# Kernel optimization log

Hardware: AMD Instinct MI355X
Metric: run time of the kernel (lower is better)

Reference implementation:

```python
import jax, jax.numpy as jnp
import numpy as np

B, C, H, W = 4, 256, 64, 64
C8 = C // 8  # q/k projection dim = 32

def setup_inputs() -> dict:
    key = jax.random.key(0)
    ks = jax.random.split(key, 6)
    s = 0.02
    return {
        "x": jax.random.normal(ks[0], (B, C, H, W), dtype=jnp.float32),
        "wq": jax.random.normal(ks[1], (C8, C), dtype=jnp.float32) * s,
        "bq": jnp.zeros((C8,), dtype=jnp.float32),
        "wk": jax.random.normal(ks[2], (C8, C), dtype=jnp.float32) * s,
        "bk": jnp.zeros((C8,), dtype=jnp.float32),
        "wv": jax.random.normal(ks[3], (C, C), dtype=jnp.float32) * s,
        "bv": jnp.zeros((C,), dtype=jnp.float32),
        "wo": jax.random.normal(ks[4], (C, C), dtype=jnp.float32) * s,
        "bo": jnp.zeros((C,), dtype=jnp.float32),
        "scale": jnp.zeros((1,), dtype=jnp.float32),
    }

def reference(x, wq, bq, wk, bk, wv, bv, wo, bo, scale):
    b, c, h, w = x.shape
    n = h * w
    xf = x.reshape(b, c, n)  # (B, C, N)
    # 1x1 convs are channel-mixing GEMMs
    q = jnp.einsum('oc,bcn->bon', wq, xf) + bq[None, :, None]  # (B, C8, N)
    k = jnp.einsum('oc,bcn->bon', wk, xf) + bk[None, :, None]  # (B, C8, N)
    v = jnp.einsum('oc,bcn->bon', wv, xf) + bv[None, :, None]  # (B, C,  N)
    inv_sqrt = 1.0 / jnp.sqrt(jnp.asarray(c // 8, dtype=x.dtype))
    scores = jnp.einsum('bon,bom->bnm', q, k) * inv_sqrt  # (B, N, N): query n, key m
    attn = jax.nn.softmax(scores, axis=-1)
    # torch: bmm(value, attn^T) -> attended[:, :, n] = sum_m v[:, :, m] * attn[n, m]
    attended = jnp.einsum('bcm,bnm->bcn', v, attn)  # (B, C, N)
    out = jnp.einsum('oc,bcn->bon', wo, attended) + bo[None, :, None]
    out = out.reshape(b, c, h, w)
    return x + scale[0] * out
```

## Files before the change

### kernel.cpp

```cpp
#include <hip/hip_runtime.h>
#include <stdint.h>

#define B_ 4
#define C_ 256
#define C8_ 32
#define N_ 4096
#define LOG2E 1.4426950408889634f
#define INV_SQRT32 0.17677669529663689f
#define QSCALE (INV_SQRT32 * LOG2E)

typedef __bf16 bf16x8 __attribute__((ext_vector_type(8)));
typedef float f32x16 __attribute__((ext_vector_type(16)));
typedef unsigned int uint4v __attribute__((ext_vector_type(4)));

__device__ __forceinline__ uint16_t f2bf(float f) {
  uint32_t u = __builtin_bit_cast(uint32_t, f);
  return (uint16_t)((u + 0x7FFFu + ((u >> 16) & 1u)) >> 16);
}
__device__ __forceinline__ uint32_t pack2bf(float a, float b) {
  uint32_t ua = __builtin_bit_cast(uint32_t, a);
  uint32_t ub = __builtin_bit_cast(uint32_t, b);
  ua = (ua + 0x7FFFu + ((ua >> 16) & 1u)) >> 16;
  ub = (ub + 0x7FFFu + ((ub >> 16) & 1u)) & 0xFFFF0000u;
  return ua | ub;
}
__device__ __forceinline__ bf16x8 load_bf8(const uint16_t* p) {
  uint4v u = *(const uint4v*)p;
  return __builtin_bit_cast(bf16x8, u);
}
__device__ __forceinline__ f32x16 mfma32(bf16x8 a, bf16x8 b, f32x16 c) {
  return __builtin_amdgcn_mfma_f32_32x32x16_bf16(a, b, c, 0, 0, 0);
}
__device__ __forceinline__ f32x16 mfma32_f8(long a, long b, f32x16 c) {
  return __builtin_amdgcn_mfma_f32_32x32x16_fp8_fp8(a, b, c, 0, 0, 0);
}

__device__ __forceinline__ void pack_p_fp8(const float* P, int h, long& pa, long& pb) {
  uint32_t w0 = __builtin_amdgcn_cvt_pk_fp8_f32(P[0], P[1], 0, false);
  w0 = __builtin_amdgcn_cvt_pk_fp8_f32(P[2], P[3], w0, true);
  uint32_t w1 = __builtin_amdgcn_cvt_pk_fp8_f32(P[4], P[5], 0, false);
  w1 = __builtin_amdgcn_cvt_pk_fp8_f32(P[6], P[7], w1, true);
  uint32_t w2 = __builtin_amdgcn_cvt_pk_fp8_f32(P[8], P[9], 0, false);
  w2 = __builtin_amdgcn_cvt_pk_fp8_f32(P[10], P[11], w2, true);
  uint32_t w3 = __builtin_amdgcn_cvt_pk_fp8_f32(P[12], P[13], 0, false);
  w3 = __builtin_amdgcn_cvt_pk_fp8_f32(P[14], P[15], w3, true);
  uint32_t s0 = h ? w0 : w1;
  uint32_t s1 = h ? w2 : w3;
  uint32_t r0 = (uint32_t)__shfl_xor((int)s0, 32, 64);
  uint32_t r1 = (uint32_t)__shfl_xor((int)s1, 32, 64);
  uint32_t a0lo = h ? r0 : w0, a0hi = h ? w1 : r0;
  uint32_t a1lo = h ? r1 : w2, a1hi = h ? w3 : r1;
  pa = (long)(((uint64_t)a0hi << 32) | a0lo);
  pb = (long)(((uint64_t)a1hi << 32) | a1lo);
}

__global__ void k_wcast(const float* __restrict__ wq, const float* __restrict__ wk,
                        const float* __restrict__ wv, const float* __restrict__ wo,
                        uint16_t* __restrict__ wqb, uint16_t* __restrict__ wkb,
                        uint16_t* __restrict__ wvb, uint16_t* __restrict__ wob) {
  int i = blockIdx.x * 256 + threadIdx.x;
  if (i < 8192) {
    int o = i >> 8, c = i & 255;
    wqb[((size_t)(c >> 3) * 32 + o) * 8 + (c & 7)] = f2bf(wq[i]);
  } else if (i < 16384) {
    int j = i - 8192; int o = j >> 8, c = j & 255;
    wkb[((size_t)(c >> 3) * 32 + o) * 8 + (c & 7)] = f2bf(wk[j]);
  } else if (i < 81920) {
    int j = i - 16384; int o = j >> 8, c = j & 255;
    wvb[((size_t)(c >> 3) * 256 + o) * 8 + (c & 7)] = f2bf(wv[j]);
  } else {
    int j = i - 81920; int o = j >> 8, c = j & 255;
    wob[((size_t)(c >> 3) * 256 + o) * 8 + (c & 7)] = f2bf(wo[j]);
  }
}

__global__ __launch_bounds__(320) void k_proj_qkv(
    const float* __restrict__ x,
    const uint16_t* __restrict__ wqb, const float* __restrict__ bq,
    const uint16_t* __restrict__ wkb, const float* __restrict__ bk,
    const uint16_t* __restrict__ wvb, const float* __restrict__ bv,
    uint16_t* __restrict__ Qb, uint16_t* __restrict__ Kt, uint8_t* __restrict__ V8) {
  __shared__ uint4v xTv[32 * 32];
  int b = blockIdx.y;
  int n0 = blockIdx.x * 32;
  int tid = threadIdx.x;
  uint16_t* xT = (uint16_t*)xTv;

  if (tid < 256) {
    int r = tid >> 3;
    int l4 = (tid & 7) * 4;
#pragma unroll
    for (int p = 0; p < 8; p++) {
      int c = p * 32 + r;
      float4 v = *(const float4*)(x + ((size_t)b * C_ + c) * N_ + n0 + l4);
      int cg = c >> 3, cj = c & 7;
      xT[(cg * 32 + l4 + 0) * 8 + cj] = f2bf(v.x);
      xT[(cg * 32 + l4 + 1) * 8 + cj] = f2bf(v.y);
      xT[(cg * 32 + l4 + 2) * 8 + cj] = f2bf(v.z);
      xT[(cg * 32 + l4 + 3) * 8 + cj] = f2bf(v.w);
    }
  }
  __syncthreads();

  int wave = tid >> 6;
  int lane = tid & 63;
  int h = lane >> 5, ln = lane & 31;

  if (wave == 0) {
    f32x16 aq, ak;
#pragma unroll
    for (int i = 0; i < 16; i++) { aq[i] = 0.0f; ak[i] = 0.0f; }
#pragma unroll 4
    for (int c = 0; c < C_; c += 16) {
      bf16x8 bb = __builtin_bit_cast(bf16x8, xTv[(c / 8 + h) * 32 + ln]);
      aq = mfma32(load_bf8(wqb + ((size_t)(c / 8 + h) * 32 + ln) * 8), bb, aq);
      ak = mfma32(load_bf8(wkb + ((size_t)(c / 8 + h) * 32 + ln) * 8), bb, ak);
    }
#pragma unroll
    for (int g = 0; g < 4; g++) {
      int row = g * 8 + h * 4;
      uint2 pq, pk;
      pq.x = pack2bf((aq[4 * g + 0] + bq[row + 0]) * QSCALE,
                     (aq[4 * g + 1] + bq[row + 1]) * QSCALE);
      pq.y = pack2bf((aq[4 * g + 2] + bq[row + 2]) * QSCALE,
                     (aq[4 * g + 3] + bq[row + 3]) * QSCALE);
      *(uint2*)(Qb + ((size_t)b * N_ + n0 + ln) * C8_ + row) = pq;
      pk.x = pack2bf(ak[4 * g + 0] + bk[row + 0], ak[4 * g + 1] + bk[row + 1]);
      pk.y = pack2bf(ak[4 * g + 2] + bk[row + 2], ak[4 * g + 3] + bk[row + 3]);
      *(uint2*)(Kt + ((size_t)(b * 4 + g) * N_ + n0 + ln) * 8 + h * 4) = pk;
    }
  } else {
    int o0 = (wave - 1) * 64;
    f32x16 a0, a1;
#pragma unroll
    for (int i = 0; i < 16; i++) { a0[i] = 0.0f; a1[i] = 0.0f; }
#pragma unroll 4
    for (int c = 0; c < C_; c += 16) {
      bf16x8 bb = __builtin_bit_cast(bf16x8, xTv[(c / 8 + h) * 32 + ln]);
      a0 = mfma32(load_bf8(wvb + ((size_t)(c / 8 + h) * 256 + o0 + ln) * 8), bb, a0);
      a1 = mfma32(load_bf8(wvb + ((size_t)(c / 8 + h) * 256 + o0 + 32 + ln) * 8), bb, a1);
    }
    int kg = b * 512 + (n0 >> 3) + (ln >> 3);
    int j = ln & 7;
#pragma unroll
    for (int r = 0; r < 16; r++) {
      int row = (r & 3) + 8 * (r >> 2) + 4 * h;
      float v0 = a0[r] + bv[o0 + row];
      float v1 = a1[r] + bv[o0 + 32 + row];
      int p0 = __builtin_amdgcn_cvt_pk_fp8_f32(v0, v0, 0, false);
      int p1 = __builtin_amdgcn_cvt_pk_fp8_f32(v1, v1, 0, false);
      V8[((size_t)kg * 256 + o0 + row) * 8 + j] = (uint8_t)(p0 & 0xff);
      V8[((size_t)kg * 256 + o0 + 32 + row) * 8 + j] = (uint8_t)(p1 & 0xff);
    }
  }
}

__global__ __launch_bounds__(512, 4) void k_attn(
    const uint16_t* __restrict__ Qb, const uint16_t* __restrict__ Kt,
    const uint8_t* __restrict__ V8, const uint16_t* __restrict__ Wob,
    const float* __restrict__ bo, const float* __restrict__ x,
    const float* __restrict__ scale, float* __restrict__ out) {
  __shared__ uint32_t sO[8][2][8][64];
  __shared__ uint4v aTv[32 * 32];
  __shared__ float sl[4][32];

  int bx = blockIdx.x;
  int b = bx >> 1;
  int qt = blockIdx.y + 64 * (bx & 1);
  int wave = threadIdx.x >> 6;
  int kw = wave >> 1, cw = wave & 1;
  int lane = threadIdx.x & 63;
  int h = lane >> 5, ln = lane & 31;
  int qi = qt * 32 + ln;

  const uint16_t* qrow = Qb + ((size_t)b * N_ + qi) * C8_;
  bf16x8 qf1 = load_bf8(qrow + h * 8);
  bf16x8 qf2 = load_bf8(qrow + 16 + h * 8);
  const uint16_t* k1base = Kt + ((size_t)(b * 4 + h) * N_) * 8;
  const uint16_t* k2base = Kt + ((size_t)(b * 4 + 2 + h) * N_) * 8;

  f32x16 O[4];
#pragma unroll
  for (int t = 0; t < 4; t++)
#pragma unroll
    for (int r = 0; r < 16; r++) O[t][r] = 0.0f;
  float lsum = 0.0f;
  const uint8_t* vbase = V8 + (size_t)(b * 512) * 2048 + cw * 1024 + ln * 8;

  int m_lo = kw * 1024;
  bf16x8 ka1 = load_bf8(k1base + (size_t)(m_lo + ln) * 8);
  bf16x8 ka2 = load_bf8(k2base + (size_t)(m_lo + ln) * 8);

  for (int m0 = m_lo; m0 < m_lo + 1024; m0 += 32) {
    int mp = (m0 + 32) & (N_ - 1);
    bf16x8 kn1 = load_bf8(k1base + (size_t)(mp + ln) * 8);
    bf16x8 kn2 = load_bf8(k2base + (size_t)(mp + ln) * 8);

    f32x16 S;
#pragma unroll
    for (int i = 0; i < 16; i++) S[i] = 0.0f;
    S = mfma32(ka1, qf1, S);
    S = mfma32(ka2, qf2, S);

    float P[16];
#pragma unroll
    for (int r = 0; r < 16; r++) {
      P[r] = __builtin_amdgcn_exp2f(fminf(S[r], 7.5f));
    }
    if (cw == 0) {
#pragma unroll
      for (int r = 0; r < 16; r++) lsum += P[r];
    }
    long pa, pb;
    pack_p_fp8(P, h, pa, pb);

    const uint8_t* vp = vbase + (size_t)((m0 >> 3) + h) * 2048;
#pragma unroll
    for (int t = 0; t < 4; t++) {
      uint2 u1 = *(const uint2*)(vp + t * 256);
      uint2 u2 = *(const uint2*)(vp + 4096 + t * 256);
      long va = (long)(((uint64_t)u1.y << 32) | u1.x);
      long vc = (long)(((uint64_t)u2.y << 32) | u2.x);
      O[t] = mfma32_f8(va, pa, O[t]);
      O[t] = mfma32_f8(vc, pb, O[t]);
    }
    ka1 = kn1; ka2 = kn2;
  }
  if (cw == 0) {
    lsum += __shfl_xor(lsum, 32, 64);
    if (h == 0) sl[kw][ln] = lsum;
  }

#pragma unroll
  for (int rr = 0; rr < 2; rr++) {
    if (rr) __syncthreads();
#pragma unroll
    for (int t2 = 0; t2 < 2; t2++) {
      int t = rr * 2 + t2;
#pragma unroll
      for (int i = 0; i < 8; i++)
        sO[wave][t2][i][lane] = pack2bf(O[t][2 * i], O[t][2 * i + 1]);
    }
    __syncthreads();
    if (wave < 4) {
      int cw2 = wave >> 1, t2 = wave & 1;
      int gt = cw2 * 4 + rr * 2 + t2;
      float acc[16];
#pragma unroll
      for (int r = 0; r < 16; r++) acc[r] = 0.0f;
#pragma unroll
      for (int k = 0; k < 4; k++) {
        int src = k * 2 + cw2;
#pragma unroll
        for (int i = 0; i < 8; i++) {
          uint32_t u = sO[src][t2][i][lane];
          acc[2 * i]     += __builtin_bit_cast(float, u << 16);
          acc[2 * i + 1] += __builtin_bit_cast(float, u & 0xFFFF0000u);
        }
      }
      float lg = sl[0][ln] + sl[1][ln] + sl[2][ln] + sl[3][ln];
      float inv = 1.0f / lg;
      uint2* aT2 = (uint2*)aTv;
#pragma unroll
      for (int g = 0; g < 4; g++) {
        uint2 pr;
        pr.x = pack2bf(acc[4 * g + 0] * inv, acc[4 * g + 1] * inv);
        pr.y = pack2bf(acc[4 * g + 2] * inv, acc[4 * g + 3] * inv);
        aT2[((gt * 4 + g) * 32 + ln) * 2 + h] = pr;
      }
    }
  }
  __syncthreads();

  int o0 = wave * 32;
  f32x16 acc;
#pragma unroll
  for (int i = 0; i < 16; i++) acc[i] = 0.0f;
#pragma unroll 4
  for (int c = 0; c < C_; c += 16) {
    bf16x8 a = load_bf8(Wob + ((size_t)(c / 8 + h) * 256 + o0 + ln) * 8);
    bf16x8 bb = __builtin_bit_cast(bf16x8, aTv[(c / 8 + h) * 32 + ln]);
    acc = mfma32(a, bb, acc);
  }
  float s = scale[0];
#pragma unroll
  for (int r = 0; r < 16; r++) {
    int row = (r & 3) + 8 * (r >> 2) + 4 * h;
    int o = o0 + row;
    size_t idx = ((size_t)b * C_ + o) * N_ + qi;
    out[idx] = x[idx] + s * (acc[r] + bo[o]);
  }
}

extern "C" void kernel_launch(void* const* d_in, const int* in_sizes, int n_in,
                              void* d_out, int out_size, void* d_ws, size_t ws_size,
                              hipStream_t stream) {
  const float* x  = (const float*)d_in[0];
  const float* wq = (const float*)d_in[1];
  const float* bq = (const float*)d_in[2];
  const float* wk = (const float*)d_in[3];
  const float* bk = (const float*)d_in[4];
  const float* wv = (const float*)d_in[5];
  const float* bv = (const float*)d_in[6];
  const float* wo = (const float*)d_in[7];
  const float* bo = (const float*)d_in[8];
  const float* scale = (const float*)d_in[9];
  float* out = (float*)d_out;

  char* w = (char*)d_ws;
  uint16_t* Qb  = (uint16_t*)(w);
  uint16_t* Kt  = (uint16_t*)(w + (1u << 20));
  uint8_t*  V8  = (uint8_t*)(w + (2u << 20));
  uint16_t* Wqb = (uint16_t*)(w + (6u << 20));
  uint16_t* Wkb = Wqb + 32 * 256;
  uint16_t* Wvb = Wkb + 32 * 256;
  uint16_t* Wob = Wvb + 256 * 256;

  k_wcast<<<576, 256, 0, stream>>>(wq, wk, wv, wo, Wqb, Wkb, Wvb, Wob);
  k_proj_qkv<<<dim3(N_ / 32, B_), 320, 0, stream>>>(x, Wqb, bq, Wkb, bk, Wvb, bv,
                                                    Qb, Kt, V8);
  k_attn<<<dim3(8, 64), 512, 0, stream>>>(Qb, Kt, V8, Wob, bo, x, scale, out);
}
```

Measured before the change: 153.4 us.

## Stagger key-tile order per wave, prefetch V earlier, vectorize x transpose stores

The attention loop now starts each wave at a different phase within its 1024-key range (staggered by wave and batch parity) so concurrent waves hit different K/V addresses. V tile loads are issued before the QK MFMA and exp so their latency overlaps compute. The projection kernel's x transpose now packs 8 channels per thread into one 16-byte LDS store instead of scalar 2-byte scattered stores, at the cost of strided scalar global loads of x. More live registers for the prefetched V may affect occupancy.

New measurement: 180.9 us. 1.18x slower.

```diff
diff --git a/kernel.cpp b/kernel.cpp
--- a/kernel.cpp
+++ b/kernel.cpp
@@ -84,20 +84,21 @@
   int b = blockIdx.y;
   int n0 = blockIdx.x * 32;
   int tid = threadIdx.x;
-  uint16_t* xT = (uint16_t*)xTv;
 
   if (tid < 256) {
-    int r = tid >> 3;
-    int l4 = (tid & 7) * 4;
-#pragma unroll
-    for (int p = 0; p < 8; p++) {
-      int c = p * 32 + r;
-      float4 v = *(const float4*)(x + ((size_t)b * C_ + c) * N_ + n0 + l4);
-      int cg = c >> 3, cj = c & 7;
-      xT[(cg * 32 + l4 + 0) * 8 + cj] = f2bf(v.x);
-      xT[(cg * 32 + l4 + 1) * 8 + cj] = f2bf(v.y);
-      xT[(cg * 32 + l4 + 2) * 8 + cj] = f2bf(v.z);
-      xT[(cg * 32 + l4 + 3) * 8 + cj] = f2bf(v.w);
+    int n = tid & 31;
+    int cg0 = tid >> 5;
+#pragma unroll
+    for (int j = 0; j < 4; j++) {
+      int cg = cg0 * 4 + j;
+      const float* xp = x + ((size_t)b * C_ + cg * 8) * N_ + n0 + n;
+      float v[8];
+#pragma unroll
+      for (int c = 0; c < 8; c++) v[c] = xp[(size_t)c * N_];
+      uint4v o;
+#pragma unroll
+      for (int p = 0; p < 4; p++) o[p] = pack2bf(v[2 * p], v[2 * p + 1]);
+      xTv[cg * 32 + n] = o;
     }
   }
   __syncthreads();
@@ -188,13 +189,24 @@
   const uint8_t* vbase = V8 + (size_t)(b * 512) * 2048 + cw * 1024 + ln * 8;
 
   int m_lo = kw * 1024;
-  bf16x8 ka1 = load_bf8(k1base + (size_t)(m_lo + ln) * 8);
-  bf16x8 ka2 = load_bf8(k2base + (size_t)(m_lo + ln) * 8);
-
-  for (int m0 = m_lo; m0 < m_lo + 1024; m0 += 32) {
-    int mp = (m0 + 32) & (N_ - 1);
+  int phase = wave * 4 + (blockIdx.y & 1) * 2;
+  int m0f = m_lo + ((phase & 31) << 5);
+  bf16x8 ka1 = load_bf8(k1base + (size_t)(m0f + ln) * 8);
+  bf16x8 ka2 = load_bf8(k2base + (size_t)(m0f + ln) * 8);
+
+  for (int it = 0; it < 32; it++) {
+    int m0 = m_lo + (((it + phase) & 31) << 5);
+    int mp = m_lo + (((it + 1 + phase) & 31) << 5);
     bf16x8 kn1 = load_bf8(k1base + (size_t)(mp + ln) * 8);
     bf16x8 kn2 = load_bf8(k2base + (size_t)(mp + ln) * 8);
+
+    const uint8_t* vp = vbase + (size_t)((m0 >> 3) + h) * 2048;
+    uint2 u1[4], u2[4];
+#pragma unroll
+    for (int t = 0; t < 4; t++) {
+      u1[t] = *(const uint2*)(vp + t * 256);
+      u2[t] = *(const uint2*)(vp + 4096 + t * 256);
+    }
 
     f32x16 S;
 #pragma unroll
@@ -214,13 +226,10 @@
     long pa, pb;
     pack_p_fp8(P, h, pa, pb);
 
-    const uint8_t* vp = vbase + (size_t)((m0 >> 3) + h) * 2048;
 #pragma unroll
     for (int t = 0; t < 4; t++) {
-      uint2 u1 = *(const uint2*)(vp + t * 256);
-      uint2 u2 = *(const uint2*)(vp + 4096 + t * 256);
-      long va = (long)(((uint64_t)u1.y << 32) | u1.x);
-      long vc = (long)(((uint64_t)u2.y << 32) | u2.x);
+      long va = (long)(((uint64_t)u1[t].y << 32) | u1[t].x);
+      long vc = (long)(((uint64_t)u2[t].y << 32) | u2[t].x);
       O[t] = mfma32_f8(va, pa, O[t]);
       O[t] = mfma32_f8(vc, pb, O[t]);
     }
```
